# Kernel tuning notes

Hardware: AMD Instinct MI355X
Metric: run time of the kernel (lower is better)

Reference implementation:

```python
import math
import jax, jax.numpy as jnp
import numpy as np

B, N, C = 2, 2048, 1024
H = 16
D = C // H  # 64
LN_EPS = 1e-5


def setup_inputs() -> dict:
    key = jax.random.key(0)
    ks = jax.random.split(key, 5)
    x = jax.random.normal(ks[0], (B, N, C), dtype=jnp.float32)
    w_qkv = jax.random.normal(ks[1], (C, 3 * C), dtype=jnp.float32) * 0.02
    w_proj = jax.random.normal(ks[2], (C, C), dtype=jnp.float32) * 0.02
    b_proj = jnp.zeros((C,), dtype=jnp.float32)
    ln_w = jnp.ones((D,), dtype=jnp.float32) + jax.random.normal(ks[3], (D,), dtype=jnp.float32) * 0.02
    ln_b = jax.random.normal(ks[4], (D,), dtype=jnp.float32) * 0.02
    return {"x": x, "w_qkv": w_qkv, "w_proj": w_proj, "b_proj": b_proj,
            "ln_w": ln_w, "ln_b": ln_b}


def _layernorm(t, w, b):
    mu = jnp.mean(t, axis=-1, keepdims=True)
    var = jnp.var(t, axis=-1, keepdims=True)
    return (t - mu) * jax.lax.rsqrt(var + LN_EPS) * w + b


def reference(x, w_qkv, w_proj, b_proj, ln_w, ln_b):
    b, n, c = x.shape
    h, d = H, c // H
    # QKV projection (no bias): [b,n,3c] -> [3,b,h,n,d]
    qkv = (x @ w_qkv).reshape(b, n, 3, h, d).transpose(2, 0, 3, 1, 4)
    q, k, v = qkv[0], qkv[1], qkv[2]
    # per-head LayerNorm on q and k (qk_norm)
    q = _layernorm(q, ln_w, ln_b)
    k = _layernorm(k, ln_w, ln_b)
    # NOTE: source multiplies q by sqrt(head_dim) (faithful to original)
    q = q * jnp.asarray(math.sqrt(d), dtype=q.dtype)
    scores = jnp.einsum('bhnd,bhmd->bhnm', q, k)  # [b,h,n,n]
    mask_value = -jnp.finfo(scores.dtype).max
    causal = jnp.tril(jnp.ones((n, n), dtype=bool))
    scores = jnp.where(causal, scores, mask_value)
    attn = jax.nn.softmax(scores, axis=-1)
    out = jnp.einsum('bhnm,bhmd->bhnd', attn, v)  # [b,h,n,d]
    out = out.transpose(0, 2, 1, 3).reshape(b, n, c)  # b n (h d)
    return out @ w_proj + b_proj
```

## Files before the change

kernel.cpp:

```cpp
#include <hip/hip_runtime.h>

#define LOG2E 1.4426950408889634f

typedef _Float16 f16x8_t __attribute__((ext_vector_type(8)));
typedef _Float16 f16x4_t __attribute__((ext_vector_type(4)));
typedef float    f32x4_t __attribute__((ext_vector_type(4)));

#define MFMA32(a, b, c) __builtin_amdgcn_mfma_f32_16x16x32_f16(a, b, c, 0, 0, 0)
#define MFMA16(a, b, c) __builtin_amdgcn_mfma_f32_16x16x16f16(a, b, c, 0, 0, 0)

__device__ __forceinline__ void async_copy16(void* lds, const void* g) {
    __builtin_amdgcn_global_load_lds(
        (const __attribute__((address_space(1))) unsigned char*)g,
        (__attribute__((address_space(3))) unsigned char*)lds, 16, 0, 0);
}

__global__ void cast_f32_f16_k(const float* __restrict__ in, _Float16* __restrict__ out, int n4) {
    int i = blockIdx.x * blockDim.x + threadIdx.x;
    if (i >= n4) return;
    float4 v = ((const float4*)in)[i];
    f16x4_t o = { (_Float16)v.x, (_Float16)v.y, (_Float16)v.z, (_Float16)v.w };
    ((f16x4_t*)out)[i] = o;
}

__global__ void transpose_cast_k(const float* __restrict__ in, _Float16* __restrict__ out,
                                 int R, int C) {
    __shared__ _Float16 tl[64][65];
    const int t = threadIdx.x;
    const int c = t & 63;
    const int r4 = t >> 6;
    const int r0 = blockIdx.y * 64, c0 = blockIdx.x * 64;
#pragma unroll
    for (int i = 0; i < 16; ++i) {
        int r = r4 + i * 4;
        tl[c][r] = (_Float16)in[(size_t)(r0 + r) * C + c0 + c];
    }
    __syncthreads();
#pragma unroll
    for (int i = 0; i < 16; ++i) {
        int rr = r4 + i * 4;
        out[(size_t)(c0 + rr) * R + r0 + c] = tl[rr][c];
    }
}

template <typename OutT, bool BIAS>
__global__ __launch_bounds__(256, 2)
void gemm_f16_k(const _Float16* __restrict__ A, const _Float16* __restrict__ BT,
                OutT* __restrict__ C, const float* __restrict__ bias,
                int M, int N, int K) {
    __shared__ _Float16 As[2][128][32];
    __shared__ _Float16 Bs[2][128][32];
    const int tid = threadIdx.x;
    const int wid = tid >> 6, lane = tid & 63;
    const int qd = lane >> 4, ln = lane & 15;
    const int m0 = blockIdx.x * 128, n0 = blockIdx.y * 128;
    const int wm = (wid >> 1) * 64, wn = (wid & 1) * 64;

    f32x4_t acc[4][4] = {};

    const int srow = lane >> 2;
    const int skk  = (lane & 3) * 8;

    for (int k0 = 0; k0 < K; k0 += 64) {
        __syncthreads();
#pragma unroll
        for (int p = 0; p < 4; ++p) {
            const int seg = p * 4 + wid;
            const int s   = seg >> 3;
            const int rg  = seg & 7;
            const int row = rg * 16 + srow;
            const size_t goff = (size_t)row * K + k0 + s * 32 + skk;
            async_copy16(&As[0][0][0] + seg * 512, A  + (size_t)m0 * K + goff);
            async_copy16(&Bs[0][0][0] + seg * 512, BT + (size_t)n0 * K + goff);
        }
        __syncthreads();
#pragma unroll
        for (int s = 0; s < 2; ++s) {
            f16x8_t a[4], b[4];
#pragma unroll
            for (int i = 0; i < 4; ++i)
                a[i] = *(const f16x8_t*)&As[s][wm + i * 16 + ln][qd * 8];
#pragma unroll
            for (int j = 0; j < 4; ++j)
                b[j] = *(const f16x8_t*)&Bs[s][wn + j * 16 + ln][qd * 8];
#pragma unroll
            for (int i = 0; i < 4; ++i)
#pragma unroll
                for (int j = 0; j < 4; ++j)
                    acc[i][j] = MFMA32(a[i], b[j], acc[i][j]);
        }
    }
#pragma unroll
    for (int i = 0; i < 4; ++i)
#pragma unroll
        for (int j = 0; j < 4; ++j) {
            const int col = n0 + wn + j * 16 + ln;
            const float bv = BIAS ? bias[col] : 0.0f;
#pragma unroll
            for (int r = 0; r < 4; ++r) {
                const int row = m0 + wm + i * 16 + qd * 4 + r;
                C[(size_t)row * N + col] = (OutT)(acc[i][j][r] + bv);
            }
        }
}

__global__ void ln_qkv_k(const _Float16* __restrict__ qkv, const float* __restrict__ ln_w,
                         const float* __restrict__ ln_b, _Float16* __restrict__ Qb,
                         _Float16* __restrict__ Kb, _Float16* __restrict__ Vb) {
    const int tid = threadIdx.x;
    const int wid = tid >> 6, lane = tid & 63;
    const int row = blockIdx.x * 4 + wid;
    const int t = row >> 4;
    const int h = row & 15;
    const int b = t >> 11, n = t & 2047;
    const size_t base = (size_t)t * 3072 + h * 64 + lane;
    float q = (float)qkv[base];
    float k = (float)qkv[base + 1024];
    float v = (float)qkv[base + 2048];
    const float wv = ln_w[lane], bv = ln_b[lane];

    float sq = q, sk = k;
#pragma unroll
    for (int m = 1; m < 64; m <<= 1) { sq += __shfl_xor(sq, m); sk += __shfl_xor(sk, m); }
    sq *= (1.0f / 64.0f); sk *= (1.0f / 64.0f);
    const float dq = q - sq, dk = k - sk;
    float vq = dq * dq, vk = dk * dk;
#pragma unroll
    for (int m = 1; m < 64; m <<= 1) { vq += __shfl_xor(vq, m); vk += __shfl_xor(vk, m); }
    vq *= (1.0f / 64.0f); vk *= (1.0f / 64.0f);
    const float yq = dq * rsqrtf(vq + 1e-5f) * wv + bv;
    const float yk = dk * rsqrtf(vk + 1e-5f) * wv + bv;
    const size_t obase = ((size_t)((b * 16 + h) * 2048 + n)) * 64 + lane;
    Qb[obase] = (_Float16)(yq * (8.0f * LOG2E));
    Kb[obase] = (_Float16)yk;
    Vb[obase] = (_Float16)v;
}

__global__ __launch_bounds__(256, 2)
void attn_k(const _Float16* __restrict__ Q, const _Float16* __restrict__ K,
            const _Float16* __restrict__ V, _Float16* __restrict__ O) {
    __shared__ _Float16 Ks[2][64][32];
    __shared__ _Float16 VT[64][64];

    const int tid = threadIdx.x;
    const int wid = tid >> 6, lane = tid & 63;
    const int qd = lane >> 4, ln = lane & 15;
    const int bh = blockIdx.x;
    const int b = bh >> 4, h = bh & 15;
    const int lob = blockIdx.y;
    const int hib = 31 - lob;
    const size_t kvbase = (size_t)bh * 2048 * 64;
    const int qh0 = hib * 64 + wid * 16;
    const int ql0 = lob * 64 + wid * 16;

    f16x8_t qfh[2], qfl[2];
#pragma unroll
    for (int s = 0; s < 2; ++s) {
        qfh[s] = *(const f16x8_t*)&Q[kvbase + (size_t)(qh0 + ln) * 64 + s * 32 + qd * 8];
        qfl[s] = *(const f16x8_t*)&Q[kvbase + (size_t)(ql0 + ln) * 64 + s * 32 + qd * 8];
    }

    f32x4_t oh[4] = {}, olo[4] = {};
    float mh = -3.0e38f, ml = -3.0e38f;
    float lh = 0.0f, ll = 0.0f;

    const int nst = hib + 1;

    for (int st = 0; st < nst; ++st) {
        const int kv0 = st * 64;
        __syncthreads();
#pragma unroll
        for (int p = 0; p < 2; ++p) {
            const int seg = p * 4 + wid;
            const int oh_ = seg * 512;
            const int hidx = oh_ + lane * 8;
            const int s_ = hidx >> 11;
            const int rrow = (hidx >> 5) & 63;
            const int kk = hidx & 31;
            async_copy16((_Float16*)Ks + oh_,
                         K + kvbase + (size_t)(kv0 + rrow) * 64 + s_ * 32 + kk);
        }
#pragma unroll
        for (int e = 0; e < 2; ++e) {
            const int idx = tid + e * 256;
            const int kv = idx & 63;
            const int d0 = (idx >> 6) * 8;
            f16x8_t vv = *(const f16x8_t*)&V[kvbase + (size_t)(kv0 + kv) * 64 + d0];
#pragma unroll
            for (int j = 0; j < 8; ++j) {
                const int d = d0 + j;
                const int col = (((kv >> 2) ^ (d & 15)) << 2) | (kv & 3);
                VT[d][col] = vv[j];
            }
        }
        __syncthreads();

        f16x8_t kb[4][2];
#pragma unroll
        for (int jt = 0; jt < 4; ++jt)
#pragma unroll
            for (int s = 0; s < 2; ++s)
                kb[jt][s] = *(const f16x8_t*)&Ks[s][jt * 16 + ln][qd * 8];
        f16x4_t vf[4][4];
#pragma unroll
        for (int dt = 0; dt < 4; ++dt)
#pragma unroll
            for (int c = 0; c < 4; ++c)
                vf[dt][c] = *(const f16x4_t*)&VT[dt * 16 + ln][(((c * 4 + qd) ^ ln) << 2)];

        auto process = [&](const f16x8_t (&qf)[2], f32x4_t (&o)[4], float& m, float& l,
                           int q0w, bool diag) {
            f32x4_t sc[4];
#pragma unroll
            for (int jt = 0; jt < 4; ++jt) {
                f32x4_t s = {};
                s = MFMA32(kb[jt][0], qf[0], s);
                s = MFMA32(kb[jt][1], qf[1], s);
                sc[jt] = s;
            }
            if (diag) {
                const int qq = q0w + ln;
#pragma unroll
                for (int c = 0; c < 4; ++c)
#pragma unroll
                    for (int r = 0; r < 4; ++r)
                        if (kv0 + c * 16 + qd * 4 + r > qq) sc[c][r] = -3.0e38f;
            }
            float mx = sc[0][0];
#pragma unroll
            for (int c = 0; c < 4; ++c)
#pragma unroll
                for (int r = 0; r < 4; ++r) mx = fmaxf(mx, sc[c][r]);
            mx = fmaxf(mx, __shfl_xor(mx, 16));
            mx = fmaxf(mx, __shfl_xor(mx, 32));
            const float mn = fmaxf(m, mx);
            const float al = exp2f(m - mn);
            m = mn;
            float rs = 0.0f;
            f16x4_t pf[4];
#pragma unroll
            for (int c = 0; c < 4; ++c)
#pragma unroll
                for (int r = 0; r < 4; ++r) {
                    const float p = exp2f(sc[c][r] - mn);
                    rs += p;
                    pf[c][r] = (_Float16)p;
                }
            l = l * al + rs;
#pragma unroll
            for (int dt = 0; dt < 4; ++dt) o[dt] *= al;
#pragma unroll
            for (int dt = 0; dt < 4; ++dt)
#pragma unroll
                for (int c = 0; c < 4; ++c)
                    o[dt] = MFMA16(vf[dt][c], pf[c], o[dt]);
        };

        process(qfh, oh, mh, lh, qh0, st == hib);
        if (st <= lob) process(qfl, olo, ml, ll, ql0, st == lob);
    }

    auto epi = [&](f32x4_t (&o)[4], float l, int q0w) {
        float t = l + __shfl_xor(l, 16);
        t = t + __shfl_xor(t, 32);
        const float inv = 1.0f / t;
        const size_t base = ((size_t)(b * 2048 + q0w + ln)) * 1024 + h * 64 + qd * 4;
#pragma unroll
        for (int dt = 0; dt < 4; ++dt) {
            f16x4_t ov;
#pragma unroll
            for (int r = 0; r < 4; ++r) ov[r] = (_Float16)(o[dt][r] * inv);
            *(f16x4_t*)&O[base + dt * 16] = ov;
        }
    };
    epi(oh, lh, qh0);
    epi(olo, ll, ql0);
}

extern "C" void kernel_launch(void* const* d_in, const int* in_sizes, int n_in,
                              void* d_out, int out_size, void* d_ws, size_t ws_size,
                              hipStream_t stream) {
    const float* x      = (const float*)d_in[0];
    const float* w_qkv  = (const float*)d_in[1];
    const float* w_proj = (const float*)d_in[2];
    const float* b_proj = (const float*)d_in[3];
    const float* ln_w   = (const float*)d_in[4];
    const float* ln_b   = (const float*)d_in[5];
    float* out = (float*)d_out;

    char* w = (char*)d_ws;
    _Float16*  qkv    = (_Float16*)w;  w += (size_t)4096 * 3072 * 2;
    _Float16*  xh     = (_Float16*)w;  w += (size_t)4096 * 1024 * 2;
    _Float16*  wqkvT  = (_Float16*)w;  w += (size_t)3072 * 1024 * 2;
    _Float16*  wprojT = (_Float16*)w;  w += (size_t)1024 * 1024 * 2;
    _Float16*  Qb     = (_Float16*)w;  w += (size_t)32 * 2048 * 64 * 2;
    _Float16*  Kb     = (_Float16*)w;  w += (size_t)32 * 2048 * 64 * 2;
    _Float16*  Vb     = (_Float16*)w;  w += (size_t)32 * 2048 * 64 * 2;
    _Float16*  Ah     = (_Float16*)w;  w += (size_t)4096 * 1024 * 2;

    cast_f32_f16_k<<<4096, 256, 0, stream>>>(x, xh, 4096 * 1024 / 4);
    transpose_cast_k<<<dim3(48, 16), 256, 0, stream>>>(w_qkv, wqkvT, 1024, 3072);
    transpose_cast_k<<<dim3(16, 16), 256, 0, stream>>>(w_proj, wprojT, 1024, 1024);
    gemm_f16_k<_Float16, false><<<dim3(32, 24), 256, 0, stream>>>(xh, wqkvT, qkv, nullptr, 4096, 3072, 1024);
    ln_qkv_k<<<16384, 256, 0, stream>>>(qkv, ln_w, ln_b, Qb, Kb, Vb);
    attn_k<<<dim3(32, 16), 256, 0, stream>>>(Qb, Kb, Vb, Ah);
    gemm_f16_k<float, true><<<dim3(32, 8), 256, 0, stream>>>(Ah, wprojT, out, b_proj, 4096, 1024, 1024);
}
```

Baseline: 211.8 us.

## Pre-transpose V globally, split attention blocks to 128 threads, smaller-tile output GEMM

Adds a kernel that writes V transposed per head into global memory, so the attention kernel can fetch V tiles with async global-to-LDS copies instead of scattered per-element LDS stores. Attention blocks now use 2 waves, and each query-block pair is split into two halves, doubling the grid to improve occupancy and load balance. The output projection gets a 64-row tile GEMM so more blocks are launched. The costs are an extra launch, an extra pass over V, and each attention block re-reading K/V for fewer queries.

Result: slower. 234.1 us (+10.5%).

```diff
diff --git a/kernel.cpp b/kernel.cpp
--- a/kernel.cpp
+++ b/kernel.cpp
@@ -40,6 +40,27 @@
     for (int i = 0; i < 16; ++i) {
         int rr = r4 + i * 4;
         out[(size_t)(c0 + rr) * R + r0 + c] = tl[rr][c];
+    }
+}
+
+__global__ void vtrans_k(const _Float16* __restrict__ qkv, _Float16* __restrict__ VTg) {
+    __shared__ _Float16 tl[64][65];
+    const int t = threadIdx.x;
+    const int bh = blockIdx.x;
+    const int b = bh >> 4, h = bh & 15;
+    const int n0 = blockIdx.y * 64;
+    const int c = t & 63;
+    const int r4 = t >> 6;
+#pragma unroll
+    for (int i = 0; i < 16; ++i) {
+        int r = r4 + i * 4;
+        tl[c][r] = qkv[(size_t)(b * 2048 + n0 + r) * 3072 + 2048 + h * 64 + c];
+    }
+    __syncthreads();
+#pragma unroll
+    for (int i = 0; i < 16; ++i) {
+        int d = r4 + i * 4;
+        VTg[(size_t)bh * 131072 + (size_t)d * 2048 + n0 + c] = tl[d][c];
     }
 }
 
@@ -104,9 +125,77 @@
         }
 }
 
-__global__ void ln_qkv_k(const _Float16* __restrict__ qkv, const float* __restrict__ ln_w,
-                         const float* __restrict__ ln_b, _Float16* __restrict__ Qb,
-                         _Float16* __restrict__ Kb, _Float16* __restrict__ Vb) {
+__global__ __launch_bounds__(256, 2)
+void gemm_f16_m64_k(const _Float16* __restrict__ A, const _Float16* __restrict__ BT,
+                    float* __restrict__ C, const float* __restrict__ bias,
+                    int M, int N, int K) {
+    __shared__ _Float16 As[2][64][32];
+    __shared__ _Float16 Bs[2][128][32];
+    const int tid = threadIdx.x;
+    const int wid = tid >> 6, lane = tid & 63;
+    const int qd = lane >> 4, ln = lane & 15;
+    const int m0 = blockIdx.x * 64, n0 = blockIdx.y * 128;
+    const int wn = wid * 32;
+
+    f32x4_t acc[4][2] = {};
+    const int srow = lane >> 2;
+    const int skk  = (lane & 3) * 8;
+
+    for (int k0 = 0; k0 < K; k0 += 64) {
+        __syncthreads();
+#pragma unroll
+        for (int p = 0; p < 2; ++p) {
+            const int seg = p * 4 + wid;
+            const int hidx = seg * 512 + lane * 8;
+            const int s_ = hidx >> 11;
+            const int row = (hidx >> 5) & 63;
+            const int kk = hidx & 31;
+            async_copy16(&As[0][0][0] + seg * 512,
+                         A + (size_t)(m0 + row) * K + k0 + s_ * 32 + kk);
+        }
+#pragma unroll
+        for (int p = 0; p < 4; ++p) {
+            const int seg = p * 4 + wid;
+            const int s   = seg >> 3;
+            const int rg  = seg & 7;
+            const int row = rg * 16 + srow;
+            async_copy16(&Bs[0][0][0] + seg * 512,
+                         BT + (size_t)(n0 + row) * K + k0 + s * 32 + skk);
+        }
+        __syncthreads();
+#pragma unroll
+        for (int s = 0; s < 2; ++s) {
+            f16x8_t a[4], b[2];
+#pragma unroll
+            for (int i = 0; i < 4; ++i)
+                a[i] = *(const f16x8_t*)&As[s][i * 16 + ln][qd * 8];
+#pragma unroll
+            for (int j = 0; j < 2; ++j)
+                b[j] = *(const f16x8_t*)&Bs[s][wn + j * 16 + ln][qd * 8];
+#pragma unroll
+            for (int i = 0; i < 4; ++i)
+#pragma unroll
+                for (int j = 0; j < 2; ++j)
+                    acc[i][j] = MFMA32(a[i], b[j], acc[i][j]);
+        }
+    }
+#pragma unroll
+    for (int i = 0; i < 4; ++i)
+#pragma unroll
+        for (int j = 0; j < 2; ++j) {
+            const int col = n0 + wn + j * 16 + ln;
+            const float bv = bias[col];
+#pragma unroll
+            for (int r = 0; r < 4; ++r) {
+                const int row = m0 + i * 16 + qd * 4 + r;
+                C[(size_t)row * N + col] = acc[i][j][r] + bv;
+            }
+        }
+}
+
+__global__ void ln_qk_k(const _Float16* __restrict__ qkv, const float* __restrict__ ln_w,
+                        const float* __restrict__ ln_b, _Float16* __restrict__ Qb,
+                        _Float16* __restrict__ Kb) {
     const int tid = threadIdx.x;
     const int wid = tid >> 6, lane = tid & 63;
     const int row = blockIdx.x * 4 + wid;
@@ -116,7 +205,6 @@
     const size_t base = (size_t)t * 3072 + h * 64 + lane;
     float q = (float)qkv[base];
     float k = (float)qkv[base + 1024];
-    float v = (float)qkv[base + 2048];
     const float wv = ln_w[lane], bv = ln_b[lane];
 
     float sq = q, sk = k;
@@ -133,12 +221,11 @@
     const size_t obase = ((size_t)((b * 16 + h) * 2048 + n)) * 64 + lane;
     Qb[obase] = (_Float16)(yq * (8.0f * LOG2E));
     Kb[obase] = (_Float16)yk;
-    Vb[obase] = (_Float16)v;
-}
-
-__global__ __launch_bounds__(256, 2)
+}
+
+__global__ __launch_bounds__(128, 3)
 void attn_k(const _Float16* __restrict__ Q, const _Float16* __restrict__ K,
-            const _Float16* __restrict__ V, _Float16* __restrict__ O) {
+            const _Float16* __restrict__ VTg, _Float16* __restrict__ O) {
     __shared__ _Float16 Ks[2][64][32];
     __shared__ _Float16 VT[64][64];
 
@@ -147,11 +234,13 @@
     const int qd = lane >> 4, ln = lane & 15;
     const int bh = blockIdx.x;
     const int b = bh >> 4, h = bh & 15;
-    const int lob = blockIdx.y;
-    const int hib = 31 - lob;
+    const int pr = blockIdx.y >> 1;
+    const int half = blockIdx.y & 1;
+    const int hib = 31 - pr, lob = pr;
     const size_t kvbase = (size_t)bh * 2048 * 64;
-    const int qh0 = hib * 64 + wid * 16;
-    const int ql0 = lob * 64 + wid * 16;
+    const size_t vtbase = (size_t)bh * 131072;
+    const int qh0 = hib * 64 + half * 32 + wid * 16;
+    const int ql0 = lob * 64 + half * 32 + wid * 16;
 
     f16x8_t qfh[2], qfl[2];
 #pragma unroll
@@ -164,14 +253,17 @@
     float mh = -3.0e38f, ml = -3.0e38f;
     float lh = 0.0f, ll = 0.0f;
 
+    const int vrow = (lane >> 3);
+    const int vY   = (lane & 7) ^ (vrow & 7);
+
     const int nst = hib + 1;
 
     for (int st = 0; st < nst; ++st) {
         const int kv0 = st * 64;
         __syncthreads();
 #pragma unroll
-        for (int p = 0; p < 2; ++p) {
-            const int seg = p * 4 + wid;
+        for (int p = 0; p < 4; ++p) {
+            const int seg = p * 2 + wid;
             const int oh_ = seg * 512;
             const int hidx = oh_ + lane * 8;
             const int s_ = hidx >> 11;
@@ -181,17 +273,11 @@
                          K + kvbase + (size_t)(kv0 + rrow) * 64 + s_ * 32 + kk);
         }
 #pragma unroll
-        for (int e = 0; e < 2; ++e) {
-            const int idx = tid + e * 256;
-            const int kv = idx & 63;
-            const int d0 = (idx >> 6) * 8;
-            f16x8_t vv = *(const f16x8_t*)&V[kvbase + (size_t)(kv0 + kv) * 64 + d0];
-#pragma unroll
-            for (int j = 0; j < 8; ++j) {
-                const int d = d0 + j;
-                const int col = (((kv >> 2) ^ (d & 15)) << 2) | (kv & 3);
-                VT[d][col] = vv[j];
-            }
+        for (int p = 0; p < 4; ++p) {
+            const int seg = p * 2 + wid;
+            const int d = seg * 8 + vrow;
+            async_copy16(&VT[0][0] + seg * 512,
+                         VTg + vtbase + (size_t)d * 2048 + kv0 + vY * 8);
         }
         __syncthreads();
 
@@ -206,7 +292,8 @@
         for (int dt = 0; dt < 4; ++dt)
 #pragma unroll
             for (int c = 0; c < 4; ++c)
-                vf[dt][c] = *(const f16x4_t*)&VT[dt * 16 + ln][(((c * 4 + qd) ^ ln) << 2)];
+                vf[dt][c] = *(const f16x4_t*)
+                    &VT[dt * 16 + ln][(((2 * c + (qd >> 1)) ^ (ln & 7)) << 3) + (qd & 1) * 4];
 
         auto process = [&](const f16x8_t (&qf)[2], f32x4_t (&o)[4], float& m, float& l,
                            int q0w, bool diag) {
@@ -295,14 +382,15 @@
     _Float16*  wprojT = (_Float16*)w;  w += (size_t)1024 * 1024 * 2;
     _Float16*  Qb     = (_Float16*)w;  w += (size_t)32 * 2048 * 64 * 2;
     _Float16*  Kb     = (_Float16*)w;  w += (size_t)32 * 2048 * 64 * 2;
-    _Float16*  Vb     = (_Float16*)w;  w += (size_t)32 * 2048 * 64 * 2;
+    _Float16*  VTg    = (_Float16*)w;  w += (size_t)32 * 64 * 2048 * 2;
     _Float16*  Ah     = (_Float16*)w;  w += (size_t)4096 * 1024 * 2;
 
     cast_f32_f16_k<<<4096, 256, 0, stream>>>(x, xh, 4096 * 1024 / 4);
     transpose_cast_k<<<dim3(48, 16), 256, 0, stream>>>(w_qkv, wqkvT, 1024, 3072);
     transpose_cast_k<<<dim3(16, 16), 256, 0, stream>>>(w_proj, wprojT, 1024, 1024);
     gemm_f16_k<_Float16, false><<<dim3(32, 24), 256, 0, stream>>>(xh, wqkvT, qkv, nullptr, 4096, 3072, 1024);
-    ln_qkv_k<<<16384, 256, 0, stream>>>(qkv, ln_w, ln_b, Qb, Kb, Vb);
-    attn_k<<<dim3(32, 16), 256, 0, stream>>>(Qb, Kb, Vb, Ah);
-    gemm_f16_k<float, true><<<dim3(32, 8), 256, 0, stream>>>(Ah, wprojT, out, b_proj, 4096, 1024, 1024);
-}
+    vtrans_k<<<dim3(32, 32), 256, 0, stream>>>(qkv, VTg);
+    ln_qk_k<<<16384, 256, 0, stream>>>(qkv, ln_w, ln_b, Qb, Kb);
+    attn_k<<<dim3(32, 32), 128, 0, stream>>>(Qb, Kb, VTg, Ah);
+    gemm_f16_m64_k<<<dim3(64, 8), 256, 0, stream>>>(Ah, wprojT, out, b_proj, 4096, 1024, 1024);
+}
```
